# Optimization experiments

Measured on AMD Instinct MI355X. Metric: run time of the kernel, lower is better.

Reference implementation:

```python
import jax, jax.numpy as jnp
import numpy as np

N = 20000       # nodes
E = 640000      # random edges (self-loops appended -> E + N total)
G = 64          # graphs in batch
F_IN = 114
H1 = 3          # heads in layer 1
D2 = 128        # output_dim of layer 2
NEG = 0.2       # GATConv leaky_relu negative slope


def setup_inputs() -> dict:
    key = jax.random.key(0)
    ks = jax.random.split(key, 20)
    x = jax.random.normal(ks[0], (N, F_IN), jnp.float32)
    src = jax.random.randint(ks[1], (E,), 0, N, jnp.int32)
    dst = jax.random.randint(ks[2], (E,), 0, N, jnp.int32)
    loop = jnp.arange(N, dtype=jnp.int32)  # PyG add_self_loops=True
    edge_index = jnp.stack([jnp.concatenate([src, loop]),
                            jnp.concatenate([dst, loop])])
    batch = (jnp.arange(N) * G // N).astype(jnp.int32)  # every graph non-empty

    def lin(k, i, o):
        return jax.random.normal(k, (i, o), jnp.float32) * (1.0 / np.sqrt(i))

    return {
        "x": x, "edge_index": edge_index, "batch": batch,
        # GATConv 1: 114 -> 114 per head, 3 heads, concat
        "W1": lin(ks[3], F_IN, H1 * F_IN),
        "a_src1": jax.random.normal(ks[4], (H1, F_IN), jnp.float32) * 0.1,
        "a_dst1": jax.random.normal(ks[5], (H1, F_IN), jnp.float32) * 0.1,
        "b1": jnp.zeros((H1 * F_IN,), jnp.float32),
        # GATConv 2: 342 -> 128, 1 head
        "W2": lin(ks[6], H1 * F_IN, D2),
        "a_src2": jax.random.normal(ks[7], (1, D2), jnp.float32) * 0.1,
        "a_dst2": jax.random.normal(ks[8], (1, D2), jnp.float32) * 0.1,
        "b2": jnp.zeros((D2,), jnp.float32),
        # MLP head
        "Wg": lin(ks[9], D2, 64),  "bg": jnp.zeros((64,), jnp.float32),
        "Wf1": lin(ks[10], 64, 32), "bf1": jnp.zeros((32,), jnp.float32),
        "Wf2": lin(ks[11], 32, 16), "bf2": jnp.zeros((16,), jnp.float32),
        "Wo": lin(ks[12], 16, 1),   "bo": jnp.zeros((1,), jnp.float32),
    }


def gat_conv(x, edge_index, W, a_src, a_dst, b, heads, dim):
    """PyG GATConv (self-loops already in edge_index, eval mode)."""
    n = x.shape[0]
    h = (x @ W).reshape(n, heads, dim)             # [N,H,D]
    src, dst = edge_index[0], edge_index[1]
    alpha_s = jnp.sum(h * a_src, axis=-1)          # [N,H]
    alpha_d = jnp.sum(h * a_dst, axis=-1)          # [N,H]
    e = jax.nn.leaky_relu(alpha_s[src] + alpha_d[dst], NEG)  # [E,H]
    # segment softmax over destination nodes
    m = jax.ops.segment_max(e, dst, num_segments=n)
    ex = jnp.exp(e - m[dst])
    s = jax.ops.segment_sum(ex, dst, num_segments=n)
    alpha = ex / s[dst]                            # [E,H]
    out = jax.ops.segment_sum(h[src] * alpha[..., None], dst, num_segments=n)
    return out.reshape(n, heads * dim) + b


def reference(x, edge_index, batch, W1, a_src1, a_dst1, b1,
              W2, a_src2, a_dst2, b2, Wg, bg, Wf1, bf1, Wf2, bf2, Wo, bo):
    h = jax.nn.elu(gat_conv(x, edge_index, W1, a_src1, a_dst1, b1, H1, F_IN))
    h = jax.nn.relu(gat_conv(h, edge_index, W2, a_src2, a_dst2, b2, 1, D2))
    g = jax.ops.segment_max(h, batch, num_segments=G)   # global max pool [G,128]
    g = jax.nn.relu(g @ Wg + bg)
    g = jax.nn.relu(g @ Wf1 + bf1)
    g = jax.nn.relu(g @ Wf2 + bf2)
    return g @ Wo + bo                                  # [G,1]
```

## Files before the change

kernel.cpp:

```cpp
#include <hip/hip_runtime.h>

#define NN 20000
#define EE 660000
#define GG 64
#define FIN 114
#define H1 3
#define F1 342
#define D2 128
#define NEG 0.2f
#define H1AS 352

__device__ inline unsigned fenc(float f) {
    unsigned u = __float_as_uint(f);
    return (u & 0x80000000u) ? ~u : (u | 0x80000000u);
}
__device__ inline float fdec(unsigned u) {
    return (u & 0x80000000u) ? __uint_as_float(u & 0x7FFFFFFFu) : __uint_as_float(~u);
}
__device__ inline float lrelu(float x) { return x > 0.f ? x : NEG * x; }

__global__ void k_wa(const float* __restrict__ W1, const float* __restrict__ aS,
                     const float* __restrict__ aD, float* __restrict__ was,
                     float* __restrict__ wad) {
    int tid = blockIdx.x * 256 + threadIdx.x;
    if (tid >= 2 * FIN * H1) return;
    int which = tid >= FIN * H1;
    int i = which ? tid - FIN * H1 : tid;
    int k = i / H1, h = i % H1;
    const float* a = which ? aD : aS;
    float s = 0.f;
    for (int d = 0; d < FIN; d++) s += W1[k * F1 + h * FIN + d] * a[h * FIN + d];
    (which ? wad : was)[i] = s;
}

__global__ void k_prep1(const float* __restrict__ W1, float* __restrict__ W1P) {
    int tid = blockIdx.x * 256 + threadIdx.x;
    if (tid >= H1 * FIN * 128) return;
    int h = tid / (FIN * 128);
    int rem = tid - h * FIN * 128;
    int k = rem / 128, c = rem % 128;
    W1P[tid] = (c < FIN) ? W1[k * F1 + h * FIN + c] : 0.f;
}

__global__ __launch_bounds__(256) void k_alpha1x(const float* __restrict__ x,
                                                 const float* __restrict__ was,
                                                 const float* __restrict__ wad,
                                                 float* __restrict__ as1,
                                                 float* __restrict__ ad1) {
    int n = blockIdx.x * 4 + (threadIdx.x >> 6);
    int l = threadIdx.x & 63;
    if (n >= NN) return;
    float x0 = x[n * FIN + l];
    float x1 = (l < FIN - 64) ? x[n * FIN + 64 + l] : 0.f;
    float s[H1], d[H1];
#pragma unroll
    for (int h = 0; h < H1; h++) {
        float w0s = was[l * H1 + h], w0d = wad[l * H1 + h];
        float w1s = (l < FIN - 64) ? was[(64 + l) * H1 + h] : 0.f;
        float w1d = (l < FIN - 64) ? wad[(64 + l) * H1 + h] : 0.f;
        s[h] = x0 * w0s + x1 * w1s;
        d[h] = x0 * w0d + x1 * w1d;
    }
#pragma unroll
    for (int o = 32; o > 0; o >>= 1) {
#pragma unroll
        for (int h = 0; h < H1; h++) {
            s[h] += __shfl_down(s[h], o);
            d[h] += __shfl_down(d[h], o);
        }
    }
    if (l == 0) {
#pragma unroll
        for (int h = 0; h < H1; h++) {
            as1[n * H1 + h] = s[h];
            ad1[n * H1 + h] = d[h];
        }
    }
}

__global__ void k_count(const int* __restrict__ dst, int* __restrict__ cnt) {
    int e = blockIdx.x * 256 + threadIdx.x;
    if (e < EE) atomicAdd(&cnt[dst[e]], 1);
}

__global__ __launch_bounds__(1024) void k_scan(const int* __restrict__ cnt,
                                               int* __restrict__ off) {
    __shared__ int part[1024];
    int t = threadIdx.x;
    const int CH = 20;
    int loc[CH];
    int s = 0;
    int base = t * CH;
    for (int i = 0; i < CH; i++) {
        int idx = base + i;
        int v = (idx < NN) ? cnt[idx] : 0;
        loc[i] = s;
        s += v;
    }
    part[t] = s;
    __syncthreads();
    for (int d = 1; d < 1024; d <<= 1) {
        int v = (t >= d) ? part[t - d] : 0;
        __syncthreads();
        part[t] += v;
        __syncthreads();
    }
    int pre = (t == 0) ? 0 : part[t - 1];
    for (int i = 0; i < CH; i++) {
        int idx = base + i;
        if (idx < NN) off[idx] = pre + loc[i];
    }
    if (t == 1023) off[NN] = part[1023];
}

__global__ void k_scatter(const int* __restrict__ src, const int* __restrict__ dst,
                          const int* __restrict__ off, int* __restrict__ cur,
                          int* __restrict__ csr_src) {
    int e = blockIdx.x * 256 + threadIdx.x;
    if (e < EE) {
        int d = dst[e];
        int pos = off[d] + atomicAdd(&cur[d], 1);
        csr_src[pos] = src[e];
    }
}

__global__ __launch_bounds__(128) void k_aggx(const float* __restrict__ x,
                                              const float* __restrict__ as1,
                                              const float* __restrict__ ad1,
                                              const int* __restrict__ off,
                                              const int* __restrict__ csr_src,
                                              float* __restrict__ xaggP) {
    int n = blockIdx.x, t = threadIdx.x;
    int e0 = off[n], e1 = off[n + 1];
    float adv0 = ad1[n * H1 + 0], adv1 = ad1[n * H1 + 1], adv2 = ad1[n * H1 + 2];
    __shared__ int ssrc[64];
    __shared__ float sw[64][H1];
    __shared__ float red[64][H1];
    float acc0 = 0.f, acc1 = 0.f, acc2 = 0.f;
    float ps0 = 0.f, ps1 = 0.f, ps2 = 0.f;
    for (int base = e0; base < e1; base += 64) {
        int c = min(64, e1 - base);
        __syncthreads();
        if (t < c) {
            int s = csr_src[base + t];
            ssrc[t] = s;
            float w0 = __expf(lrelu(as1[s * H1 + 0] + adv0));
            float w1 = __expf(lrelu(as1[s * H1 + 1] + adv1));
            float w2 = __expf(lrelu(as1[s * H1 + 2] + adv2));
            sw[t][0] = w0; sw[t][1] = w1; sw[t][2] = w2;
            ps0 += w0; ps1 += w1; ps2 += w2;
        }
        __syncthreads();
        if (t < FIN) {
            for (int j = 0; j < c; j++) {
                float xv = x[ssrc[j] * FIN + t];
                acc0 += xv * sw[j][0];
                acc1 += xv * sw[j][1];
                acc2 += xv * sw[j][2];
            }
        }
    }
    __syncthreads();
    if (t < 64) { red[t][0] = ps0; red[t][1] = ps1; red[t][2] = ps2; }
    __syncthreads();
    for (int sr = 32; sr > 0; sr >>= 1) {
        if (t < sr) {
            red[t][0] += red[t + sr][0];
            red[t][1] += red[t + sr][1];
            red[t][2] += red[t + sr][2];
        }
        __syncthreads();
    }
    float i0 = 1.f / red[0][0], i1 = 1.f / red[0][1], i2 = 1.f / red[0][2];
    float v0 = (t < FIN) ? acc0 * i0 : 0.f;
    float v1 = (t < FIN) ? acc1 * i1 : 0.f;
    float v2 = (t < FIN) ? acc2 * i2 : 0.f;
    xaggP[(size_t)0 * NN * 128 + n * 128 + t] = v0;
    xaggP[(size_t)1 * NN * 128 + n * 128 + t] = v1;
    xaggP[(size_t)2 * NN * 128 + n * 128 + t] = v2;
}

__global__ __launch_bounds__(256) void k_gemm1t(const float* __restrict__ xaggP,
                                                const float* __restrict__ W1P,
                                                const float* __restrict__ b1,
                                                float* __restrict__ h1aP) {
    int h = blockIdx.y;
    int rb = blockIdx.x * 64;
    int t = threadIdx.x;
    int tr = t >> 4, tc = t & 15;
    __shared__ float As[32][68];
    __shared__ float Bs[32][132];
    const float* Ap = xaggP + (size_t)h * NN * 128;
    const float* Bp = W1P + h * FIN * 128;
    float acc[4][8] = {};
    for (int k0 = 0; k0 < 128; k0 += 32) {
        if (k0) __syncthreads();
#pragma unroll
        for (int q = 0; q < 2; q++) {
            int idd = t + q * 256;
            int row = idd >> 3, kq = idd & 7;
            int gr = rb + row;
            float4 v = (gr < NN) ? *(const float4*)(Ap + (size_t)gr * 128 + k0 + kq * 4)
                                 : make_float4(0.f, 0.f, 0.f, 0.f);
            As[kq * 4 + 0][row] = v.x;
            As[kq * 4 + 1][row] = v.y;
            As[kq * 4 + 2][row] = v.z;
            As[kq * 4 + 3][row] = v.w;
        }
#pragma unroll
        for (int q = 0; q < 4; q++) {
            int idd = t + q * 256;
            int kk = idd >> 5, nf = idd & 31;
            int kg = k0 + kk;
            float4 v = (kg < FIN) ? *(const float4*)(Bp + kg * 128 + nf * 4)
                                  : make_float4(0.f, 0.f, 0.f, 0.f);
            *(float4*)(&Bs[kk][nf * 4]) = v;
        }
        __syncthreads();
#pragma unroll 4
        for (int k = 0; k < 32; k++) {
            float4 a = *(const float4*)(&As[k][tr * 4]);
            float4 b0 = *(const float4*)(&Bs[k][tc * 4]);
            float4 b1r = *(const float4*)(&Bs[k][64 + tc * 4]);
            float av[4] = {a.x, a.y, a.z, a.w};
            float bv[8] = {b0.x, b0.y, b0.z, b0.w, b1r.x, b1r.y, b1r.z, b1r.w};
#pragma unroll
            for (int r = 0; r < 4; r++)
#pragma unroll
                for (int j = 0; j < 8; j++) acc[r][j] += av[r] * bv[j];
        }
    }
    int hb = h * FIN;
#pragma unroll
    for (int r = 0; r < 4; r++) {
        int row = rb + tr * 4 + r;
        if (row >= NN) continue;
        float* orow = h1aP + (size_t)row * H1AS + hb;
#pragma unroll
        for (int j = 0; j < 8; j++) {
            int c = (j < 4) ? (tc * 4 + j) : (64 + tc * 4 + j - 4);
            if (c < FIN) {
                float v = acc[r][j] + b1[hb + c];
                orow[c] = v > 0.f ? v : expm1f(v);
            } else if (h == 2 && c < 124) {
                orow[c] = 0.f;
            }
        }
    }
}

__global__ __launch_bounds__(256) void k_gemm2t(const float* __restrict__ h1aP,
                                                const float* __restrict__ W2,
                                                const float* __restrict__ aS2,
                                                const float* __restrict__ aD2,
                                                float* __restrict__ h2,
                                                float* __restrict__ as2,
                                                float* __restrict__ ad2) {
    int rb = blockIdx.x * 64;
    int t = threadIdx.x;
    int tr = t >> 4, tc = t & 15;
    __shared__ float As[32][68];
    __shared__ float Bs[32][132];
    float acc[4][8] = {};
    for (int k0 = 0; k0 < H1AS; k0 += 32) {
        if (k0) __syncthreads();
#pragma unroll
        for (int q = 0; q < 2; q++) {
            int idd = t + q * 256;
            int row = idd >> 3, kq = idd & 7;
            int gr = rb + row;
            float4 v = (gr < NN) ? *(const float4*)(h1aP + (size_t)gr * H1AS + k0 + kq * 4)
                                 : make_float4(0.f, 0.f, 0.f, 0.f);
            As[kq * 4 + 0][row] = v.x;
            As[kq * 4 + 1][row] = v.y;
            As[kq * 4 + 2][row] = v.z;
            As[kq * 4 + 3][row] = v.w;
        }
#pragma unroll
        for (int q = 0; q < 4; q++) {
            int idd = t + q * 256;
            int kk = idd >> 5, nf = idd & 31;
            int kg = k0 + kk;
            float4 v = (kg < F1) ? *(const float4*)(W2 + (size_t)kg * D2 + nf * 4)
                                 : make_float4(0.f, 0.f, 0.f, 0.f);
            *(float4*)(&Bs[kk][nf * 4]) = v;
        }
        __syncthreads();
#pragma unroll 4
        for (int k = 0; k < 32; k++) {
            float4 a = *(const float4*)(&As[k][tr * 4]);
            float4 b0 = *(const float4*)(&Bs[k][tc * 4]);
            float4 b1r = *(const float4*)(&Bs[k][64 + tc * 4]);
            float av[4] = {a.x, a.y, a.z, a.w};
            float bv[8] = {b0.x, b0.y, b0.z, b0.w, b1r.x, b1r.y, b1r.z, b1r.w};
#pragma unroll
            for (int r = 0; r < 4; r++)
#pragma unroll
                for (int j = 0; j < 8; j++) acc[r][j] += av[r] * bv[j];
        }
    }
    float sA[8], sD[8];
#pragma unroll
    for (int j = 0; j < 8; j++) {
        int c = (j < 4) ? (tc * 4 + j) : (64 + tc * 4 + j - 4);
        sA[j] = aS2[c];
        sD[j] = aD2[c];
    }
#pragma unroll
    for (int r = 0; r < 4; r++) {
        int row = rb + tr * 4 + r;
        bool ok = (row < NN);
        if (ok) {
            *(float4*)(&h2[(size_t)row * D2 + tc * 4]) =
                make_float4(acc[r][0], acc[r][1], acc[r][2], acc[r][3]);
            *(float4*)(&h2[(size_t)row * D2 + 64 + tc * 4]) =
                make_float4(acc[r][4], acc[r][5], acc[r][6], acc[r][7]);
        }
        float s = 0.f, d = 0.f;
#pragma unroll
        for (int j = 0; j < 8; j++) { s += acc[r][j] * sA[j]; d += acc[r][j] * sD[j]; }
#pragma unroll
        for (int o = 8; o > 0; o >>= 1) {
            s += __shfl_xor(s, o);
            d += __shfl_xor(d, o);
        }
        if (tc == 0 && ok) {
            as2[row] = s;
            ad2[row] = d;
        }
    }
}

__global__ __launch_bounds__(128) void k_agg2f(const float* __restrict__ h2,
                                               const float* __restrict__ as2,
                                               const float* __restrict__ ad2,
                                               const int* __restrict__ off,
                                               const int* __restrict__ csr_src,
                                               const float* __restrict__ b2,
                                               float* __restrict__ h3) {
    int n = blockIdx.x, t = threadIdx.x;
    int e0 = off[n], e1 = off[n + 1];
    float adv = ad2[n];
    __shared__ int ssrc[64];
    __shared__ float sw[64];
    __shared__ float red[64];
    float acc = 0.f, ps = 0.f;
    for (int base = e0; base < e1; base += 64) {
        int c = min(64, e1 - base);
        __syncthreads();
        if (t < c) {
            int s = csr_src[base + t];
            ssrc[t] = s;
            float w = __expf(lrelu(as2[s] + adv));
            sw[t] = w;
            ps += w;
        }
        __syncthreads();
        for (int j = 0; j < c; j++) acc += h2[ssrc[j] * D2 + t] * sw[j];
    }
    __syncthreads();
    if (t < 64) red[t] = ps;
    __syncthreads();
    for (int sr = 32; sr > 0; sr >>= 1) {
        if (t < sr) red[t] += red[t + sr];
        __syncthreads();
    }
    float v = acc / red[0] + b2[t];
    h3[n * D2 + t] = fmaxf(v, 0.f);
}

__global__ __launch_bounds__(128) void k_pool(const float* __restrict__ h3,
                                              unsigned* __restrict__ poolbuf) {
    int g = blockIdx.x, part = blockIdx.y, t = threadIdx.x;
    int n0 = (g * NN + GG - 1) / GG;
    int n1 = ((g + 1) * NN + GG - 1) / GG;
    int cnt = n1 - n0, ch = (cnt + 7) / 8;
    int s0 = n0 + part * ch, s1 = min(s0 + ch, n1);
    float mx = -1e30f;
    for (int n = s0; n < s1; n++) mx = fmaxf(mx, h3[n * D2 + t]);
    if (s0 < s1) atomicMax(&poolbuf[g * D2 + t], fenc(mx));
}

__global__ __launch_bounds__(128) void k_mlp(const unsigned* __restrict__ poolbuf,
                                             const float* __restrict__ Wg,
                                             const float* __restrict__ bg,
                                             const float* __restrict__ Wf1,
                                             const float* __restrict__ bf1,
                                             const float* __restrict__ Wf2,
                                             const float* __restrict__ bf2,
                                             const float* __restrict__ Wo,
                                             const float* __restrict__ bo,
                                             float* __restrict__ out) {
    int g = blockIdx.x;
    int t = threadIdx.x;
    __shared__ float pool[D2];
    __shared__ float a1[64];
    __shared__ float a2[32];
    __shared__ float a3[16];
    pool[t] = fdec(poolbuf[g * D2 + t]);
    __syncthreads();
    if (t < 64) {
        float acc = bg[t];
        for (int k = 0; k < D2; k++) acc += pool[k] * Wg[k * 64 + t];
        a1[t] = fmaxf(acc, 0.f);
    }
    __syncthreads();
    if (t < 32) {
        float acc = bf1[t];
        for (int k = 0; k < 64; k++) acc += a1[k] * Wf1[k * 32 + t];
        a2[t] = fmaxf(acc, 0.f);
    }
    __syncthreads();
    if (t < 16) {
        float acc = bf2[t];
        for (int k = 0; k < 32; k++) acc += a2[k] * Wf2[k * 16 + t];
        a3[t] = fmaxf(acc, 0.f);
    }
    __syncthreads();
    if (t == 0) {
        float acc = bo[0];
        for (int k = 0; k < 16; k++) acc += a3[k] * Wo[k];
        out[g] = acc;
    }
}

extern "C" void kernel_launch(void* const* d_in, const int* in_sizes, int n_in,
                              void* d_out, int out_size, void* d_ws, size_t ws_size,
                              hipStream_t stream) {
    const float* x = (const float*)d_in[0];
    const int* ei = (const int*)d_in[1];
    const float* W1 = (const float*)d_in[3];
    const float* aS1 = (const float*)d_in[4];
    const float* aD1 = (const float*)d_in[5];
    const float* b1 = (const float*)d_in[6];
    const float* W2 = (const float*)d_in[7];
    const float* aS2 = (const float*)d_in[8];
    const float* aD2 = (const float*)d_in[9];
    const float* b2 = (const float*)d_in[10];
    const float* Wg = (const float*)d_in[11];
    const float* bg = (const float*)d_in[12];
    const float* Wf1 = (const float*)d_in[13];
    const float* bf1 = (const float*)d_in[14];
    const float* Wf2 = (const float*)d_in[15];
    const float* bf2 = (const float*)d_in[16];
    const float* Wo = (const float*)d_in[17];
    const float* bo = (const float*)d_in[18];
    float* out = (float*)d_out;

    const int* src = ei;
    const int* dst = ei + EE;

    char* ws = (char*)d_ws;
    size_t o = 0;
    auto alloc = [&](size_t bytes) -> char* {
        char* p = ws + o;
        o += (bytes + 255) & ~(size_t)255;
        return p;
    };
    float* was = (float*)alloc((size_t)FIN * H1 * 4);
    float* wad = (float*)alloc((size_t)FIN * H1 * 4);
    float* W1P = (float*)alloc((size_t)H1 * FIN * 128 * 4);
    float* as1 = (float*)alloc((size_t)NN * H1 * 4);
    float* ad1 = (float*)alloc((size_t)NN * H1 * 4);
    int* cnt = (int*)alloc((size_t)NN * 4);
    int* off = (int*)alloc((size_t)(NN + 1) * 4);
    int* cur = (int*)alloc((size_t)NN * 4);
    int* csr_src = (int*)alloc((size_t)EE * 4);
    float* xaggP = (float*)alloc((size_t)H1 * NN * 128 * 4);
    float* h1aP = (float*)alloc((size_t)NN * H1AS * 4);
    float* h2 = (float*)alloc((size_t)NN * D2 * 4);
    float* as2 = (float*)alloc((size_t)NN * 4);
    float* ad2 = (float*)alloc((size_t)NN * 4);
    float* h3 = (float*)alloc((size_t)NN * D2 * 4);
    unsigned* poolbuf = (unsigned*)alloc((size_t)GG * D2 * 4);
    (void)ws_size;

    hipMemsetAsync(cnt, 0, (size_t)NN * 4, stream);
    hipMemsetAsync(cur, 0, (size_t)NN * 4, stream);
    hipMemsetAsync(poolbuf, 0, (size_t)GG * D2 * 4, stream);

    const int EB = (EE + 255) / 256;

    k_wa<<<(2 * FIN * H1 + 255) / 256, 256, 0, stream>>>(W1, aS1, aD1, was, wad);
    k_prep1<<<(H1 * FIN * 128 + 255) / 256, 256, 0, stream>>>(W1, W1P);
    k_alpha1x<<<(NN + 3) / 4, 256, 0, stream>>>(x, was, wad, as1, ad1);
    k_count<<<EB, 256, 0, stream>>>(dst, cnt);
    k_scan<<<1, 1024, 0, stream>>>(cnt, off);
    k_scatter<<<EB, 256, 0, stream>>>(src, dst, off, cur, csr_src);
    k_aggx<<<NN, 128, 0, stream>>>(x, as1, ad1, off, csr_src, xaggP);
    k_gemm1t<<<dim3((NN + 63) / 64, H1), 256, 0, stream>>>(xaggP, W1P, b1, h1aP);
    k_gemm2t<<<(NN + 63) / 64, 256, 0, stream>>>(h1aP, W2, aS2, aD2, h2, as2, ad2);
    k_agg2f<<<NN, 128, 0, stream>>>(h2, as2, ad2, off, csr_src, b2, h3);
    k_pool<<<dim3(GG, 8), 128, 0, stream>>>(h3, poolbuf);
    k_mlp<<<GG, 128, 0, stream>>>(poolbuf, Wg, bg, Wf1, bf1, Wf2, bf2, Wo, bo, out);
}
```

Measured before the change: 299.7 us.

## Register-prefetch GEMM tiles, split gemm2 columns, fuse pooling into aggregation

Both GEMM kernels now stage the next K tile in registers while computing the current one, and store A row-major with vector reads. The weight pad is extended so the K-bound checks go away. gemm2 is split into two 64-column halves to double the block count, and its attention dot products move into a separate k_alpha2 kernel. Global max pooling is fused into k_agg2f through per-node atomicMax, which removes the h3 buffer and the k_pool pass, at the cost of many atomics contending on the same pool entries.

```diff
diff --git a/kernel.cpp b/kernel.cpp
--- a/kernel.cpp
+++ b/kernel.cpp
@@ -35,11 +35,11 @@
 
 __global__ void k_prep1(const float* __restrict__ W1, float* __restrict__ W1P) {
     int tid = blockIdx.x * 256 + threadIdx.x;
-    if (tid >= H1 * FIN * 128) return;
-    int h = tid / (FIN * 128);
-    int rem = tid - h * FIN * 128;
-    int k = rem / 128, c = rem % 128;
-    W1P[tid] = (c < FIN) ? W1[k * F1 + h * FIN + c] : 0.f;
+    if (tid >= H1 * 128 * 128) return;
+    int h = tid / (128 * 128);
+    int rem = tid & (128 * 128 - 1);
+    int k = rem >> 7, c = rem & 127;
+    W1P[tid] = (c < FIN && k < FIN) ? W1[k * F1 + h * FIN + c] : 0.f;
 }
 
 __global__ __launch_bounds__(256) void k_alpha1x(const float* __restrict__ x,
@@ -188,46 +188,63 @@
     int rb = blockIdx.x * 64;
     int t = threadIdx.x;
     int tr = t >> 4, tc = t & 15;
-    __shared__ float As[32][68];
+    __shared__ float As[64][36];
     __shared__ float Bs[32][132];
     const float* Ap = xaggP + (size_t)h * NN * 128;
-    const float* Bp = W1P + h * FIN * 128;
+    const float* Bp = W1P + (size_t)h * 128 * 128;
+    const float4 zf4 = make_float4(0.f, 0.f, 0.f, 0.f);
+
+    int ar0 = t >> 3, ak0 = t & 7;
+    int ar1 = 32 + ar0;
+    int bk[4], bn[4];
+#pragma unroll
+    for (int q = 0; q < 4; q++) { int idd = t + q * 256; bk[q] = idd >> 5; bn[q] = idd & 31; }
+
+    float4 aR[2], bR[4];
+    {
+        int g0 = rb + ar0, g1 = rb + ar1;
+        aR[0] = (g0 < NN) ? *(const float4*)(Ap + (size_t)g0 * 128 + ak0 * 4) : zf4;
+        aR[1] = (g1 < NN) ? *(const float4*)(Ap + (size_t)g1 * 128 + ak0 * 4) : zf4;
+#pragma unroll
+        for (int q = 0; q < 4; q++)
+            bR[q] = *(const float4*)(Bp + (size_t)bk[q] * 128 + bn[q] * 4);
+    }
     float acc[4][8] = {};
-    for (int k0 = 0; k0 < 128; k0 += 32) {
-        if (k0) __syncthreads();
-#pragma unroll
-        for (int q = 0; q < 2; q++) {
-            int idd = t + q * 256;
-            int row = idd >> 3, kq = idd & 7;
-            int gr = rb + row;
-            float4 v = (gr < NN) ? *(const float4*)(Ap + (size_t)gr * 128 + k0 + kq * 4)
-                                 : make_float4(0.f, 0.f, 0.f, 0.f);
-            As[kq * 4 + 0][row] = v.x;
-            As[kq * 4 + 1][row] = v.y;
-            As[kq * 4 + 2][row] = v.z;
-            As[kq * 4 + 3][row] = v.w;
-        }
-#pragma unroll
-        for (int q = 0; q < 4; q++) {
-            int idd = t + q * 256;
-            int kk = idd >> 5, nf = idd & 31;
-            int kg = k0 + kk;
-            float4 v = (kg < FIN) ? *(const float4*)(Bp + kg * 128 + nf * 4)
-                                  : make_float4(0.f, 0.f, 0.f, 0.f);
-            *(float4*)(&Bs[kk][nf * 4]) = v;
-        }
-        __syncthreads();
-#pragma unroll 4
-        for (int k = 0; k < 32; k++) {
-            float4 a = *(const float4*)(&As[k][tr * 4]);
-            float4 b0 = *(const float4*)(&Bs[k][tc * 4]);
-            float4 b1r = *(const float4*)(&Bs[k][64 + tc * 4]);
-            float av[4] = {a.x, a.y, a.z, a.w};
-            float bv[8] = {b0.x, b0.y, b0.z, b0.w, b1r.x, b1r.y, b1r.z, b1r.w};
+    for (int tile = 0; tile < 4; tile++) {
+        if (tile) __syncthreads();
+        *(float4*)(&As[ar0][ak0 * 4]) = aR[0];
+        *(float4*)(&As[ar1][ak0 * 4]) = aR[1];
+#pragma unroll
+        for (int q = 0; q < 4; q++) *(float4*)(&Bs[bk[q]][bn[q] * 4]) = bR[q];
+        __syncthreads();
+        if (tile < 3) {
+            int k0 = (tile + 1) * 32;
+            int g0 = rb + ar0, g1 = rb + ar1;
+            aR[0] = (g0 < NN) ? *(const float4*)(Ap + (size_t)g0 * 128 + k0 + ak0 * 4) : zf4;
+            aR[1] = (g1 < NN) ? *(const float4*)(Ap + (size_t)g1 * 128 + k0 + ak0 * 4) : zf4;
+#pragma unroll
+            for (int q = 0; q < 4; q++)
+                bR[q] = *(const float4*)(Bp + (size_t)(k0 + bk[q]) * 128 + bn[q] * 4);
+        }
+#pragma unroll
+        for (int kc = 0; kc < 32; kc += 4) {
+            float a4[4][4];
 #pragma unroll
             for (int r = 0; r < 4; r++)
-#pragma unroll
-                for (int j = 0; j < 8; j++) acc[r][j] += av[r] * bv[j];
+                *(float4*)a4[r] = *(const float4*)(&As[tr * 4 + r][kc]);
+#pragma unroll
+            for (int kk = 0; kk < 4; kk++) {
+                float4 b0 = *(const float4*)(&Bs[kc + kk][tc * 4]);
+                float4 b1v = *(const float4*)(&Bs[kc + kk][64 + tc * 4]);
+#pragma unroll
+                for (int r = 0; r < 4; r++) {
+                    float av = a4[r][kk];
+                    acc[r][0] += av * b0.x;  acc[r][1] += av * b0.y;
+                    acc[r][2] += av * b0.z;  acc[r][3] += av * b0.w;
+                    acc[r][4] += av * b1v.x; acc[r][5] += av * b1v.y;
+                    acc[r][6] += av * b1v.z; acc[r][7] += av * b1v.w;
+                }
+            }
         }
     }
     int hb = h * FIN;
@@ -238,7 +255,7 @@
         float* orow = h1aP + (size_t)row * H1AS + hb;
 #pragma unroll
         for (int j = 0; j < 8; j++) {
-            int c = (j < 4) ? (tc * 4 + j) : (64 + tc * 4 + j - 4);
+            int c = (j < 4) ? (tc * 4 + j) : (64 + tc * 4 + (j - 4));
             if (c < FIN) {
                 float v = acc[r][j] + b1[hb + c];
                 orow[c] = v > 0.f ? v : expm1f(v);
@@ -251,83 +268,87 @@
 
 __global__ __launch_bounds__(256) void k_gemm2t(const float* __restrict__ h1aP,
                                                 const float* __restrict__ W2,
-                                                const float* __restrict__ aS2,
-                                                const float* __restrict__ aD2,
-                                                float* __restrict__ h2,
+                                                float* __restrict__ h2) {
+    int mt = blockIdx.x >> 1, nb = (blockIdx.x & 1) * 64;
+    int rb = mt * 64;
+    int t = threadIdx.x;
+    int tr = t >> 4, tc = t & 15;
+    __shared__ float As[64][36];
+    __shared__ float Bs[32][68];
+    const float4 zf4 = make_float4(0.f, 0.f, 0.f, 0.f);
+    int ar0 = t >> 3, ak0 = t & 7;
+    int ar1 = 32 + ar0;
+    int bk0 = t >> 4, bn0 = t & 15;
+    int bk1 = 16 + bk0;
+    float4 aR[2], bR[2];
+    {
+        int g0 = rb + ar0, g1 = rb + ar1;
+        aR[0] = (g0 < NN) ? *(const float4*)(h1aP + (size_t)g0 * H1AS + ak0 * 4) : zf4;
+        aR[1] = (g1 < NN) ? *(const float4*)(h1aP + (size_t)g1 * H1AS + ak0 * 4) : zf4;
+        bR[0] = *(const float4*)(W2 + (size_t)bk0 * D2 + nb + bn0 * 4);
+        bR[1] = *(const float4*)(W2 + (size_t)bk1 * D2 + nb + bn0 * 4);
+    }
+    float acc[4][4] = {};
+    for (int tile = 0; tile < 11; tile++) {
+        if (tile) __syncthreads();
+        *(float4*)(&As[ar0][ak0 * 4]) = aR[0];
+        *(float4*)(&As[ar1][ak0 * 4]) = aR[1];
+        *(float4*)(&Bs[bk0][bn0 * 4]) = bR[0];
+        *(float4*)(&Bs[bk1][bn0 * 4]) = bR[1];
+        __syncthreads();
+        if (tile < 10) {
+            int k0 = (tile + 1) * 32;
+            int g0 = rb + ar0, g1 = rb + ar1;
+            aR[0] = (g0 < NN) ? *(const float4*)(h1aP + (size_t)g0 * H1AS + k0 + ak0 * 4) : zf4;
+            aR[1] = (g1 < NN) ? *(const float4*)(h1aP + (size_t)g1 * H1AS + k0 + ak0 * 4) : zf4;
+            bR[0] = (k0 + bk0 < F1) ? *(const float4*)(W2 + (size_t)(k0 + bk0) * D2 + nb + bn0 * 4) : zf4;
+            bR[1] = (k0 + bk1 < F1) ? *(const float4*)(W2 + (size_t)(k0 + bk1) * D2 + nb + bn0 * 4) : zf4;
+        }
+#pragma unroll
+        for (int kc = 0; kc < 32; kc += 4) {
+            float a4[4][4];
+#pragma unroll
+            for (int r = 0; r < 4; r++)
+                *(float4*)a4[r] = *(const float4*)(&As[tr * 4 + r][kc]);
+#pragma unroll
+            for (int kk = 0; kk < 4; kk++) {
+                float4 b0 = *(const float4*)(&Bs[kc + kk][tc * 4]);
+#pragma unroll
+                for (int r = 0; r < 4; r++) {
+                    float av = a4[r][kk];
+                    acc[r][0] += av * b0.x; acc[r][1] += av * b0.y;
+                    acc[r][2] += av * b0.z; acc[r][3] += av * b0.w;
+                }
+            }
+        }
+    }
+#pragma unroll
+    for (int r = 0; r < 4; r++) {
+        int row = rb + tr * 4 + r;
+        if (row < NN)
+            *(float4*)(&h2[(size_t)row * D2 + nb + tc * 4]) =
+                make_float4(acc[r][0], acc[r][1], acc[r][2], acc[r][3]);
+    }
+}
+
+__global__ __launch_bounds__(256) void k_alpha2(const float* __restrict__ h2,
+                                                const float* __restrict__ aS,
+                                                const float* __restrict__ aD,
                                                 float* __restrict__ as2,
                                                 float* __restrict__ ad2) {
-    int rb = blockIdx.x * 64;
-    int t = threadIdx.x;
-    int tr = t >> 4, tc = t & 15;
-    __shared__ float As[32][68];
-    __shared__ float Bs[32][132];
-    float acc[4][8] = {};
-    for (int k0 = 0; k0 < H1AS; k0 += 32) {
-        if (k0) __syncthreads();
-#pragma unroll
-        for (int q = 0; q < 2; q++) {
-            int idd = t + q * 256;
-            int row = idd >> 3, kq = idd & 7;
-            int gr = rb + row;
-            float4 v = (gr < NN) ? *(const float4*)(h1aP + (size_t)gr * H1AS + k0 + kq * 4)
-                                 : make_float4(0.f, 0.f, 0.f, 0.f);
-            As[kq * 4 + 0][row] = v.x;
-            As[kq * 4 + 1][row] = v.y;
-            As[kq * 4 + 2][row] = v.z;
-            As[kq * 4 + 3][row] = v.w;
-        }
-#pragma unroll
-        for (int q = 0; q < 4; q++) {
-            int idd = t + q * 256;
-            int kk = idd >> 5, nf = idd & 31;
-            int kg = k0 + kk;
-            float4 v = (kg < F1) ? *(const float4*)(W2 + (size_t)kg * D2 + nf * 4)
-                                 : make_float4(0.f, 0.f, 0.f, 0.f);
-            *(float4*)(&Bs[kk][nf * 4]) = v;
-        }
-        __syncthreads();
-#pragma unroll 4
-        for (int k = 0; k < 32; k++) {
-            float4 a = *(const float4*)(&As[k][tr * 4]);
-            float4 b0 = *(const float4*)(&Bs[k][tc * 4]);
-            float4 b1r = *(const float4*)(&Bs[k][64 + tc * 4]);
-            float av[4] = {a.x, a.y, a.z, a.w};
-            float bv[8] = {b0.x, b0.y, b0.z, b0.w, b1r.x, b1r.y, b1r.z, b1r.w};
-#pragma unroll
-            for (int r = 0; r < 4; r++)
-#pragma unroll
-                for (int j = 0; j < 8; j++) acc[r][j] += av[r] * bv[j];
-        }
-    }
-    float sA[8], sD[8];
-#pragma unroll
-    for (int j = 0; j < 8; j++) {
-        int c = (j < 4) ? (tc * 4 + j) : (64 + tc * 4 + j - 4);
-        sA[j] = aS2[c];
-        sD[j] = aD2[c];
-    }
-#pragma unroll
-    for (int r = 0; r < 4; r++) {
-        int row = rb + tr * 4 + r;
-        bool ok = (row < NN);
-        if (ok) {
-            *(float4*)(&h2[(size_t)row * D2 + tc * 4]) =
-                make_float4(acc[r][0], acc[r][1], acc[r][2], acc[r][3]);
-            *(float4*)(&h2[(size_t)row * D2 + 64 + tc * 4]) =
-                make_float4(acc[r][4], acc[r][5], acc[r][6], acc[r][7]);
-        }
-        float s = 0.f, d = 0.f;
-#pragma unroll
-        for (int j = 0; j < 8; j++) { s += acc[r][j] * sA[j]; d += acc[r][j] * sD[j]; }
-#pragma unroll
-        for (int o = 8; o > 0; o >>= 1) {
-            s += __shfl_xor(s, o);
-            d += __shfl_xor(d, o);
-        }
-        if (tc == 0 && ok) {
-            as2[row] = s;
-            ad2[row] = d;
-        }
+    int n = blockIdx.x * 4 + (threadIdx.x >> 6);
+    int l = threadIdx.x & 63;
+    if (n >= NN) return;
+    float v0 = h2[(size_t)n * D2 + l], v1 = h2[(size_t)n * D2 + 64 + l];
+    float ps = v0 * aS[l] + v1 * aS[64 + l];
+    float pd = v0 * aD[l] + v1 * aD[64 + l];
+    for (int o = 32; o > 0; o >>= 1) {
+        ps += __shfl_down(ps, o);
+        pd += __shfl_down(pd, o);
+    }
+    if (l == 0) {
+        as2[n] = ps;
+        ad2[n] = pd;
     }
 }
 
@@ -337,7 +358,7 @@
                                                const int* __restrict__ off,
                                                const int* __restrict__ csr_src,
                                                const float* __restrict__ b2,
-                                               float* __restrict__ h3) {
+                                               unsigned* __restrict__ poolbuf) {
     int n = blockIdx.x, t = threadIdx.x;
     int e0 = off[n], e1 = off[n + 1];
     float adv = ad2[n];
@@ -356,7 +377,7 @@
             ps += w;
         }
         __syncthreads();
-        for (int j = 0; j < c; j++) acc += h2[ssrc[j] * D2 + t] * sw[j];
+        for (int j = 0; j < c; j++) acc += h2[(size_t)ssrc[j] * D2 + t] * sw[j];
     }
     __syncthreads();
     if (t < 64) red[t] = ps;
@@ -365,20 +386,9 @@
         if (t < sr) red[t] += red[t + sr];
         __syncthreads();
     }
-    float v = acc / red[0] + b2[t];
-    h3[n * D2 + t] = fmaxf(v, 0.f);
-}
-
-__global__ __launch_bounds__(128) void k_pool(const float* __restrict__ h3,
-                                              unsigned* __restrict__ poolbuf) {
-    int g = blockIdx.x, part = blockIdx.y, t = threadIdx.x;
-    int n0 = (g * NN + GG - 1) / GG;
-    int n1 = ((g + 1) * NN + GG - 1) / GG;
-    int cnt = n1 - n0, ch = (cnt + 7) / 8;
-    int s0 = n0 + part * ch, s1 = min(s0 + ch, n1);
-    float mx = -1e30f;
-    for (int n = s0; n < s1; n++) mx = fmaxf(mx, h3[n * D2 + t]);
-    if (s0 < s1) atomicMax(&poolbuf[g * D2 + t], fenc(mx));
+    float v = fmaxf(acc / red[0] + b2[t], 0.f);
+    int g = (int)(((long long)n * GG) / NN);
+    atomicMax(&poolbuf[g * D2 + t], fenc(v));
 }
 
 __global__ __launch_bounds__(128) void k_mlp(const unsigned* __restrict__ poolbuf,
@@ -459,7 +469,7 @@
     };
     float* was = (float*)alloc((size_t)FIN * H1 * 4);
     float* wad = (float*)alloc((size_t)FIN * H1 * 4);
-    float* W1P = (float*)alloc((size_t)H1 * FIN * 128 * 4);
+    float* W1P = (float*)alloc((size_t)H1 * 128 * 128 * 4);
     float* as1 = (float*)alloc((size_t)NN * H1 * 4);
     float* ad1 = (float*)alloc((size_t)NN * H1 * 4);
     int* cnt = (int*)alloc((size_t)NN * 4);
@@ -471,7 +481,6 @@
     float* h2 = (float*)alloc((size_t)NN * D2 * 4);
     float* as2 = (float*)alloc((size_t)NN * 4);
     float* ad2 = (float*)alloc((size_t)NN * 4);
-    float* h3 = (float*)alloc((size_t)NN * D2 * 4);
     unsigned* poolbuf = (unsigned*)alloc((size_t)GG * D2 * 4);
     (void)ws_size;
 
@@ -482,15 +491,15 @@
     const int EB = (EE + 255) / 256;
 
     k_wa<<<(2 * FIN * H1 + 255) / 256, 256, 0, stream>>>(W1, aS1, aD1, was, wad);
-    k_prep1<<<(H1 * FIN * 128 + 255) / 256, 256, 0, stream>>>(W1, W1P);
+    k_prep1<<<(H1 * 128 * 128 + 255) / 256, 256, 0, stream>>>(W1, W1P);
     k_alpha1x<<<(NN + 3) / 4, 256, 0, stream>>>(x, was, wad, as1, ad1);
     k_count<<<EB, 256, 0, stream>>>(dst, cnt);
     k_scan<<<1, 1024, 0, stream>>>(cnt, off);
     k_scatter<<<EB, 256, 0, stream>>>(src, dst, off, cur, csr_src);
     k_aggx<<<NN, 128, 0, stream>>>(x, as1, ad1, off, csr_src, xaggP);
     k_gemm1t<<<dim3((NN + 63) / 64, H1), 256, 0, stream>>>(xaggP, W1P, b1, h1aP);
-    k_gemm2t<<<(NN + 63) / 64, 256, 0, stream>>>(h1aP, W2, aS2, aD2, h2, as2, ad2);
-    k_agg2f<<<NN, 128, 0, stream>>>(h2, as2, ad2, off, csr_src, b2, h3);
-    k_pool<<<dim3(GG, 8), 128, 0, stream>>>(h3, poolbuf);
+    k_gemm2t<<<((NN + 63) / 64) * 2, 256, 0, stream>>>(h1aP, W2, h2);
+    k_alpha2<<<(NN + 3) / 4, 256, 0, stream>>>(h2, aS2, aD2, as2, ad2);
+    k_agg2f<<<NN, 128, 0, stream>>>(h2, as2, ad2, off, csr_src, b2, poolbuf);
     k_mlp<<<GG, 128, 0, stream>>>(poolbuf, Wg, bg, Wf1, bf1, Wf2, bf2, Wo, bo, out);
 }
```

Result: slower. 319.4 us (+6.6%).
